# Optimization experiments

Hardware: AMD Instinct MI355X
Metric: run time of the kernel (lower is better)

The kernel has to match this reference:

```python
import jax, jax.numpy as jnp
import numpy as np

N, M, D, DE, H, G = 2048, 16, 512, 128, 8, 50
DH, DEH, NF = D // H, DE // H, 4  # head dims; 2**2 frames for 2D frame averaging
OPS = jnp.array([[-1., -1.], [-1., 1.], [1., -1.], [1., 1.]], dtype=jnp.float32)

def ln(x, eps=1e-5):
    m = x.mean(-1, keepdims=True)
    v = x.var(-1, keepdims=True)
    return (x - m) * jax.lax.rsqrt(v + eps)

def mlp2(x, w1, b1, w2, b2):
    # timm-style Mlp with norm_layer=LayerNorm: fc1 -> GELU -> LN -> fc2 (dropout=0)
    h = jax.nn.gelu(x @ w1 + b1, approximate=False)
    return ln(h) @ w2 + b2

def setup_inputs():
    key = jax.random.key(0)
    ks = iter(jax.random.split(key, 32))
    def w(shape):
        return jax.random.normal(next(ks), shape, jnp.float32) / float(np.sqrt(shape[0]))
    return dict(
        gene_exp=jax.random.uniform(next(ks), (N, G), jnp.float32),
        token_embs=jax.random.normal(next(ks), (N, D), jnp.float32),
        coords=jax.random.uniform(next(ks), (N, 2), jnp.float32) * 100.0,
        neighbor_indices=jax.random.randint(next(ks), (N, M), 0, N),
        w_qkv=w((D, 3 * D)), b_qkv=jnp.zeros((3 * D,), jnp.float32),
        wa1=w((2 * DH + DEH + G, D)), ba1=jnp.zeros((D,), jnp.float32),
        wa2=w((D, 1)), ba2=jnp.zeros((1,), jnp.float32),
        we1=w((3, DE)), be1=jnp.zeros((DE,), jnp.float32),
        we2=w((DE, DE)), be2=jnp.zeros((DE,), jnp.float32),
        wo1=w((D + DE, D)), bo1=jnp.zeros((D,), jnp.float32),
        wo2=w((D, D)), bo2=jnp.zeros((D,), jnp.float32),
        wm1=w((D, 4 * D)), bm1=jnp.zeros((4 * D,), jnp.float32),
        wm2=w((4 * D, D)), bm2=jnp.zeros((D,), jnp.float32),
        wg1=w((D, D)), bg1=jnp.zeros((D,), jnp.float32),
        wg2=w((D, G)), bg2=jnp.zeros((G,), jnp.float32),
    )

def reference(gene_exp, token_embs, coords, neighbor_indices, w_qkv, b_qkv, wa1, ba1, wa2, ba2, we1, be1, we2, be2, wo1, bo1, wo2, bo2, wm1, bm1, wm2, bm2, wg1, bg1, wg2, bg2):
    qkv = ln(token_embs) @ w_qkv + b_qkv
    q, k, v = jnp.split(qkv, 3, axis=-1)
    q, k, v = (t.reshape(N, H, DH) for t in (q, k, v))
    # --- frame averaging over neighbor point clouds (dim=2 -> 4 sign frames) ---
    radial = coords[neighbor_indices] - coords[:, None, :]            # [N,M,2]
    rnorm = jnp.linalg.norm(radial, axis=-1, keepdims=True)           # [N,M,1]
    Xc = radial - radial.mean(axis=1, keepdims=True)
    C = jnp.einsum('nmi,nmj->nij', Xc, Xc)                            # [N,2,2]
    _, V = jnp.linalg.eigh(jax.lax.stop_gradient(C))                  # eigh on detached cov (as in torch code)
    proj = jnp.einsum('nmj,nji->nmi', Xc, V)                          # [N,M,2]
    frame = OPS[None, :, None, :] * proj[:, None, :, :]               # [N,4,M,2]
    rn = jnp.broadcast_to(rnorm[:, None], (N, NF, M, 1))
    edge = mlp2(jnp.concatenate([frame, rn], axis=-1), we1, be1, we2, be2).mean(axis=1)  # [N,M,DE]
    # --- per-edge MLP attention ---
    gd = gene_exp[neighbor_indices] - gene_exp[:, None, :]            # [N,M,G]
    msg = jnp.concatenate([
        jnp.broadcast_to(q[:, None], (N, M, H, DH)),
        k[neighbor_indices],
        edge.reshape(N, M, H, DEH),
        jnp.broadcast_to(gd[:, :, None, :], (N, M, H, G)),
    ], axis=-1)                                                       # [N,M,H,2*DH+DEH+G]
    logits = mlp2(msg, wa1, ba1, wa2, ba2)[..., 0]                    # [N,M,H]
    attn = jax.nn.softmax(logits.transpose(0, 2, 1), axis=-1)         # [N,H,M]
    # --- context aggregation ---
    sc = jnp.einsum('nhm,nmhd->nhd', attn, v[neighbor_indices]).reshape(N, D)
    ec = jnp.einsum('nhm,nmhd->nhd', attn, edge.reshape(N, M, H, DEH)).reshape(N, DE)
    ctx = mlp2(jnp.concatenate([sc, ec], axis=-1), wo1, bo1, wo2, bo2)
    tok = token_embs + ctx
    tok = tok + mlp2(tok, wm1, bm1, wm2, bm2)
    # gene updater: Linear -> GELU -> LN -> Linear
    gene_out = mlp2(tok, wg1, bg1, wg2, bg2)
    return gene_out, tok
```

## Files before the change

kernel.cpp:

```cpp
#include <hip/hip_runtime.h>
#include <math.h>

#define NN 2048
#define MM 16
#define DD 512
#define DE 128
#define HH 8
#define GG 50
#define DH 64
#define DEH 16

typedef __attribute__((ext_vector_type(8))) short bf8_t;
typedef __attribute__((ext_vector_type(4))) float f4_t;
typedef __attribute__((ext_vector_type(2))) float f2_t;
typedef unsigned short us;

__device__ __forceinline__ void gload16(const us* g, us* l) {
    __builtin_amdgcn_global_load_lds(
        (const __attribute__((address_space(1))) unsigned int*)g,
        (__attribute__((address_space(3))) unsigned int*)l, 16, 0, 0);
}

__device__ __forceinline__ float gelu_f(float x) {
    float u = 1.5957691216f * fmaf(0.044715f * x, x * x, x);
    u = fminf(fmaxf(u, -30.f), 30.f);
    float e = __expf(u);
    float t = fmaf(-2.f, __builtin_amdgcn_rcpf(e + 1.f), 1.f);
    float hx = 0.5f * x;
    return fmaf(hx, t, hx);
}

__device__ __forceinline__ f2_t gelu2(f2_t x) {
    f2_t u = ((x * 0.044715f) * (x * x) + x) * 1.5957691216f;
    f2_t e1;
    e1.x = __expf(u.x) + 1.f;
    e1.y = __expf(u.y) + 1.f;
    f2_t r;
    r.x = __builtin_amdgcn_rcpf(e1.x);
    r.y = __builtin_amdgcn_rcpf(e1.y);
    f2_t t = r * (-2.f) + 1.f;
    f2_t hx = x * 0.5f;
    return hx * t + hx;
}

__device__ __forceinline__ float wsum(float v) {
#pragma unroll
    for (int o = 32; o; o >>= 1) v += __shfl_xor(v, o, 64);
    return v;
}

__device__ __forceinline__ us f2bf(float x) {
    union { float f; unsigned int u; } v;
    v.f = x;
    unsigned int r = v.u + 0x7FFFu + ((v.u >> 16) & 1u);
    return (us)(r >> 16);
}

__device__ __forceinline__ float bfu(unsigned int u) {
    union { unsigned int x; float f; } v;
    v.x = u;
    return v.f;
}
#define BF_LO(u) bfu((u) << 16)
#define BF_HI(u) bfu((u) & 0xFFFF0000u)
__device__ __forceinline__ float b2f(us u) { return bfu((unsigned int)u << 16); }

__global__ __launch_bounds__(256) void act_ln_kernel(float* __restrict__ outF,
                                                     us* __restrict__ outB,
                                                     const float* __restrict__ x,
                                                     int C, int do_gelu) {
    int row = blockIdx.x, tid = threadIdx.x;
    int nv = C >> 8;
    float v[8];
    float s = 0.f, ss = 0.f;
    for (int i = 0; i < nv; ++i) {
        float val = x[(size_t)row * C + tid + (i << 8)];
        if (do_gelu) val = gelu_f(val);
        v[i] = val;
        s += val;
        ss += val * val;
    }
    __shared__ float red[4][2];
    s = wsum(s);
    ss = wsum(ss);
    int wid = tid >> 6, lane = tid & 63;
    if (lane == 0) { red[wid][0] = s; red[wid][1] = ss; }
    __syncthreads();
    s = red[0][0] + red[1][0] + red[2][0] + red[3][0];
    ss = red[0][1] + red[1][1] + red[2][1] + red[3][1];
    float mean = s / (float)C;
    float var = ss / (float)C - mean * mean;
    float rs = rsqrtf(var + 1e-5f);
    for (int i = 0; i < nv; ++i) {
        float y = (v[i] - mean) * rs;
        size_t idx = (size_t)row * C + tid + (i << 8);
        if (outF) outF[idx] = y;
        if (outB) outB[idx] = f2bf(y);
    }
}

__global__ __launch_bounds__(256) void combine2ln_kernel(const float* __restrict__ pk,
                                                         const float* __restrict__ bias,
                                                         us* __restrict__ outB) {
    int row = blockIdx.x, tid = threadIdx.x;
    size_t b = (size_t)row * 512;
    float v0 = gelu_f(pk[b + tid] + pk[1048576 + b + tid] + bias[tid]);
    float v1 = gelu_f(pk[b + 256 + tid] + pk[1048576 + b + 256 + tid] + bias[256 + tid]);
    __shared__ float red[4][2];
    float s = wsum(v0 + v1);
    float ss = wsum(fmaf(v0, v0, v1 * v1));
    int wid = tid >> 6, lane = tid & 63;
    if (lane == 0) { red[wid][0] = s; red[wid][1] = ss; }
    __syncthreads();
    s = red[0][0] + red[1][0] + red[2][0] + red[3][0];
    ss = red[0][1] + red[1][1] + red[2][1] + red[3][1];
    float mean = s * (1.f / 512.f);
    float var = ss * (1.f / 512.f) - mean * mean;
    float rs = rsqrtf(var + 1e-5f);
    outB[b + tid] = f2bf((v0 - mean) * rs);
    outB[b + 256 + tid] = f2bf((v1 - mean) * rs);
}

__global__ __launch_bounds__(256) void combine2_kernel(const float* __restrict__ pk,
                                                       const float* __restrict__ bias,
                                                       const float* __restrict__ resid,
                                                       float* __restrict__ outF,
                                                       us* __restrict__ outB) {
    int idx = blockIdx.x * 256 + threadIdx.x;
    float v = pk[idx] + pk[idx + 1048576] + bias[idx & 511] + resid[idx];
    outF[idx] = v;
    outB[idx] = f2bf(v);
}

__global__ __launch_bounds__(256) void wm2_combine(const float* __restrict__ pk,
                                                   const float* __restrict__ bias,
                                                   const float* __restrict__ resid,
                                                   float* __restrict__ outF,
                                                   us* __restrict__ outB) {
    int idx = blockIdx.x * 256 + threadIdx.x;
    float v = pk[idx] + pk[idx + 1048576] + pk[idx + 2097152] + pk[idx + 3145728] +
              bias[idx & 511] + resid[idx];
    outF[idx] = v;
    outB[idx] = f2bf(v);
}

__global__ __launch_bounds__(256) void wg2_combine(const float* __restrict__ pk,
                                                   const float* __restrict__ bias,
                                                   float* __restrict__ outF) {
    int idx = blockIdx.x * 256 + threadIdx.x;
    if (idx >= 102400) return;
    float v = pk[idx] + pk[idx + 102400] + pk[idx + 204800] + pk[idx + 307200] +
              bias[idx % 50];
    outF[idx] = v;
}

__global__ __launch_bounds__(256) void lnproj_kernel(const float* __restrict__ te,
                                                     us* __restrict__ x_ln_bf,
                                                     const float* __restrict__ coords,
                                                     const int* __restrict__ nbr,
                                                     float* __restrict__ projs,
                                                     float* __restrict__ rns) {
    int tid = threadIdx.x;
    if (blockIdx.x < 2048) {
        int row = blockIdx.x;
        float v0 = te[(size_t)row * 512 + tid];
        float v1 = te[(size_t)row * 512 + 256 + tid];
        __shared__ float red[4][2];
        float s = wsum(v0 + v1);
        float ss = wsum(fmaf(v0, v0, v1 * v1));
        int wid = tid >> 6, lane = tid & 63;
        if (lane == 0) { red[wid][0] = s; red[wid][1] = ss; }
        __syncthreads();
        s = red[0][0] + red[1][0] + red[2][0] + red[3][0];
        ss = red[0][1] + red[1][1] + red[2][1] + red[3][1];
        float mean = s * (1.f / 512.f);
        float var = ss * (1.f / 512.f) - mean * mean;
        float rs = rsqrtf(var + 1e-5f);
        x_ln_bf[(size_t)row * 512 + tid] = f2bf((v0 - mean) * rs);
        x_ln_bf[(size_t)row * 512 + 256 + tid] = f2bf((v1 - mean) * rs);
        return;
    }
    int node = (blockIdx.x - 2048) * 16 + (tid >> 4);
    int m = tid & 15;
    float cx = coords[node * 2], cy = coords[node * 2 + 1];
    int j = nbr[node * 16 + m];
    float rx = coords[j * 2] - cx;
    float ry = coords[j * 2 + 1] - cy;
    float rn = sqrtf(rx * rx + ry * ry);
    float mx = rx, my = ry;
#pragma unroll
    for (int o = 8; o; o >>= 1) { mx += __shfl_xor(mx, o, 16); my += __shfl_xor(my, o, 16); }
    mx *= 0.0625f;
    my *= 0.0625f;
    float xcx = rx - mx, xcy = ry - my;
    float sxx = xcx * xcx, sxy = xcx * xcy, syy = xcy * xcy;
#pragma unroll
    for (int o = 8; o; o >>= 1) {
        sxx += __shfl_xor(sxx, o, 16);
        sxy += __shfl_xor(sxy, o, 16);
        syy += __shfl_xor(syy, o, 16);
    }
    double a = (double)sxx, b = (double)sxy, c = (double)syy;
    double diff = 0.5 * (a - c);
    double disc = sqrt(diff * diff + b * b);
    double l2 = 0.5 * (a + c) + disc;
    double v2x = b, v2y = l2 - a;
    double nn2 = sqrt(v2x * v2x + v2y * v2y);
    if (nn2 < 1e-30) { v2x = (a >= c) ? 1.0 : 0.0; v2y = 1.0 - v2x; nn2 = 1.0; }
    v2x /= nn2;
    v2y /= nn2;
    double v1x = -v2y, v1y = v2x;
    int row = node * 16 + m;
    projs[row * 2] = (float)((double)xcx * v1x + (double)xcy * v1y);
    projs[row * 2 + 1] = (float)((double)xcx * v2x + (double)xcy * v2y);
    rns[row] = rn;
}

struct TCJob {
    const float* src;
    us* dst;
    int K, N, Kld, b0;
};
struct TC11 {
    TCJob j[11];
    int acc_end;
    const float* wa1_s;
    us* wesT_d;
    const float* gene_s;
    us* gene_d;
};

__global__ __launch_bounds__(256) void tcast_all(TC11 P) {
    __shared__ float tile[32][33];
    int b = blockIdx.x;
    if (b >= P.acc_end) {
        int lb = b - P.acc_end;
        if (lb < 64) {
            int idx = lb * 256 + threadIdx.x;
            int c = idx >> 5, t = idx & 31;
            P.wesT_d[idx] = (t < 16) ? f2bf(P.wa1_s[(size_t)(128 + t) * 512 + c]) : (us)0;
        } else {
            int idx = (lb - 64) * 256 + threadIdx.x;
            int r = idx >> 6, c = idx & 63;
            P.gene_d[idx] = (c < 50) ? f2bf(P.gene_s[r * 50 + c]) : (us)0;
        }
        return;
    }
    int ji = 0;
#pragma unroll
    for (int i = 1; i < 11; ++i)
        if (b >= P.j[i].b0) ji = i;
    const float* W = P.j[ji].src;
    us* Wt = P.j[ji].dst;
    int K = P.j[ji].K, N = P.j[ji].N, Kld = P.j[ji].Kld;
    int lb = b - P.j[ji].b0;
    int nbx = (N + 31) >> 5;
    int n0 = (lb % nbx) * 32, k0 = (lb / nbx) * 32;
    int tx = threadIdx.x & 31, ty = threadIdx.x >> 5;
#pragma unroll
    for (int p = 0; p < 4; ++p) {
        int k = k0 + ty + p * 8;
        tile[ty + p * 8][tx] = (k < K && n0 + tx < N) ? W[(size_t)k * N + n0 + tx] : 0.f;
    }
    __syncthreads();
#pragma unroll
    for (int p = 0; p < 4; ++p) {
        int n = n0 + ty + p * 8;
        if (n < N && k0 + tx < Kld) Wt[(size_t)n * Kld + k0 + tx] = f2bf(tile[tx][ty + p * 8]);
    }
}

struct GJob {
    const us* A;
    const us* Bt;
    const float* bias;
    const float* resid;
    const float* residH;
    float* outF;
    us* outB;
    us* outB2;
    us* outB3;
    int M, Kstride, nkt, N, Nout, b0;
};
struct GJobs {
    GJob j[4];
    int nj;
};

__global__ __launch_bounds__(256) void gemm_bf16_kernel(GJobs P) {
    __shared__ us As[2][128 * 64];
    __shared__ us Bs[2][128 * 64];
    int b = blockIdx.x;
    int ji = 0;
#pragma unroll
    for (int i = 1; i < 4; ++i)
        if (i < P.nj && b >= P.j[i].b0) ji = i;
    const us* A = P.j[ji].A;
    const us* Bt = P.j[ji].Bt;
    int Kst = P.j[ji].Kstride, nkt = P.j[ji].nkt;
    int Nn = P.j[ji].N, Nout = P.j[ji].Nout;
    int lb = b - P.j[ji].b0;
    int ncol = Nn >> 7;
    int col0 = (lb % ncol) << 7, row0 = (lb / ncol) << 7;

    int tid = threadIdx.x;
    int lane = tid & 63;
    int w = tid >> 6;
    int wr = w >> 1, wc = w & 1;
    f4_t acc[4][4];
#pragma unroll
    for (int a = 0; a < 4; ++a)
#pragma unroll
        for (int bb = 0; bb < 4; ++bb) {
            acc[a][bb][0] = 0.f; acc[a][bb][1] = 0.f;
            acc[a][bb][2] = 0.f; acc[a][bb][3] = 0.f;
        }

    auto stage = [&](int buf, int kt) {
#pragma unroll
        for (int p = 0; p < 4; ++p) {
            int id = p * 256 + tid;
            int r = id >> 3, cch = id & 7;
            int kc = cch ^ (r & 7);
            int wb = p * 256 + (tid & 192);
            gload16(A + (size_t)(row0 + r) * Kst + kt + kc * 8, As[buf] + wb * 8);
            gload16(Bt + (size_t)(col0 + r) * Kst + kt + kc * 8, Bs[buf] + wb * 8);
        }
    };

    stage(0, 0);
    __syncthreads();
    for (int t = 0; t < nkt; ++t) {
        int cur = t & 1;
        if (t + 1 < nkt) stage(cur ^ 1, (t + 1) << 6);
#pragma unroll
        for (int kk = 0; kk < 2; ++kk) {
            bf8_t af[4], bfr[4];
            int kslot = kk * 4 + (lane >> 4);
#pragma unroll
            for (int mi = 0; mi < 4; ++mi) {
                int r = wr * 64 + mi * 16 + (lane & 15);
                af[mi] = *(const bf8_t*)((char*)As[cur] + r * 128 + ((kslot ^ (r & 7)) * 16));
            }
#pragma unroll
            for (int ni = 0; ni < 4; ++ni) {
                int r = wc * 64 + ni * 16 + (lane & 15);
                bfr[ni] = *(const bf8_t*)((char*)Bs[cur] + r * 128 + ((kslot ^ (r & 7)) * 16));
            }
#pragma unroll
            for (int mi = 0; mi < 4; ++mi)
#pragma unroll
                for (int ni = 0; ni < 4; ++ni)
                    acc[mi][ni] = __builtin_amdgcn_mfma_f32_16x16x32_bf16(
                        af[mi], bfr[ni], acc[mi][ni], 0, 0, 0);
        }
        __syncthreads();
    }
    const float* bias = P.j[ji].bias;
    const float* resid = P.j[ji].resid;
    const float* residH = P.j[ji].residH;
    float* outF = P.j[ji].outF;
    us* outB = P.j[ji].outB;
    us* outB2 = P.j[ji].outB2;
    us* outB3 = P.j[ji].outB3;
    int cr = lane >> 4, cc = lane & 15;
#pragma unroll
    for (int mi = 0; mi < 4; ++mi)
#pragma unroll
        for (int ni = 0; ni < 4; ++ni) {
            int col = col0 + wc * 64 + ni * 16 + cc;
            if (col >= Nout) continue;
            float bv = bias ? bias[col] : 0.f;
#pragma unroll
            for (int j = 0; j < 4; ++j) {
                int row = row0 + wr * 64 + mi * 16 + cr * 4 + j;
                float v = acc[mi][ni][j] + bv;
                if (resid) v += resid[(size_t)row * Nout + col];
                if (residH) v += residH[(size_t)(row >> 3) * Nout + col];
                if (outF) outF[(size_t)row * Nout + col] = v;
                if (outB) {
                    if (outB2) {
                        int seg = col >> 9, cl = col & 511;
                        us* dst = seg == 0 ? outB : (seg == 1 ? outB2 : outB3);
                        dst[(size_t)row * 512 + cl] = f2bf(v);
                    } else {
                        outB[(size_t)row * Nout + col] = f2bf(v);
                    }
                }
            }
        }
}

__global__ __launch_bounds__(256) void frame_mlp1_kernel(const float* __restrict__ projs,
                                                         const float* __restrict__ rns,
                                                         const float* __restrict__ we1,
                                                         const float* __restrict__ be1,
                                                         us* __restrict__ u) {
    int row = blockIdx.x * 4 + (threadIdx.x >> 6);
    int lane = threadIdx.x & 63;
    float px = projs[row * 2], py = projs[row * 2 + 1], rn = rns[row];
    int c0 = lane, c1 = lane + 64;
    float w10a = we1[c0], w11a = we1[128 + c0], w12a = we1[256 + c0], b1a = be1[c0];
    float w10b = we1[c1], w11b = we1[128 + c1], w12b = we1[256 + c1], b1b = be1[c1];
    float acc0 = 0.f, acc1 = 0.f;
    const float opsx[4] = {-1.f, -1.f, 1.f, 1.f};
    const float opsy[4] = {-1.f, 1.f, -1.f, 1.f};
#pragma unroll
    for (int f = 0; f < 4; ++f) {
        float fx = opsx[f] * px, fy = opsy[f] * py;
        float h0 = gelu_f(fmaf(fx, w10a, fmaf(fy, w11a, fmaf(rn, w12a, b1a))));
        float h1 = gelu_f(fmaf(fx, w10b, fmaf(fy, w11b, fmaf(rn, w12b, b1b))));
        float s = wsum(h0 + h1);
        float ss = wsum(fmaf(h0, h0, h1 * h1));
        float mean = s * (1.f / 128.f);
        float var = ss * (1.f / 128.f) - mean * mean;
        float rs = rsqrtf(var + 1e-5f);
        acc0 += (h0 - mean) * rs;
        acc1 += (h1 - mean) * rs;
    }
    u[(size_t)row * 128 + c0] = f2bf(0.25f * acc0);
    u[(size_t)row * 128 + c1] = f2bf(0.25f * acc1);
}

__global__ __launch_bounds__(256) void logits_fused_kernel(
    const us* __restrict__ qpb,
    const us* __restrict__ k2b,
    const us* __restrict__ gepb,
    const us* __restrict__ edgeb,
    const us* __restrict__ wesT,
    const us* __restrict__ wa1kT,
    const int* __restrict__ nbr,
    const float* __restrict__ wa2,
    const float* __restrict__ ba2,
    const us* __restrict__ v2b,
    us* __restrict__ scec) {
    __shared__ us Es[2048 + 32];
    __shared__ us qmg[8 * 520];
    __shared__ us gepj[16 * 512];
    __shared__ float wa2s[512];
    __shared__ float lgs[128];
    __shared__ float attn[128];
    __shared__ float sinv[8];
    __shared__ int jns[16];
    int n = blockIdx.x, tid = threadIdx.x;
    int lane = tid & 63;
    float swv = 0.f;
#pragma unroll
    for (int i = 0; i < 8; ++i) swv += wa2[lane + 64 * i];
    float sw = wsum(swv);
    float ba2v = ba2[0];
    {
        const uint* s2 = (const uint*)(edgeb + (size_t)n * 2048);
        uint* d2 = (uint*)Es;
        for (int i = tid; i < 1040; i += 256) d2[i] = s2[i];
        const uint* s3 = (const uint*)(qpb + (size_t)n * 4096);
        const uint* s4 = (const uint*)(gepb + (size_t)n * 512);
        uint* d3 = (uint*)qmg;
        for (int i = tid; i < 2048; i += 256) {
            uint q = s3[i], g = s4[i & 255];
            float lo = BF_LO(q) - BF_LO(g), hi = BF_HI(q) - BF_HI(g);
            d3[(i >> 8) * 260 + (i & 255)] = ((uint)f2bf(hi) << 16) | (uint)f2bf(lo);
        }
        uint* d5 = (uint*)gepj;
#pragma unroll 4
        for (int p = 0; p < 16; ++p) {
            int j = nbr[n * 16 + p];
            d5[p * 256 + tid] = ((const uint*)(gepb + (size_t)j * 512))[tid];
        }
        for (int i = tid; i < 512; i += 256) wa2s[i] = wa2[i];
        if (tid < 16) jns[tid] = nbr[n * 16 + tid];
    }
    __syncthreads();

    int cc = lane & 15, cr = lane >> 4;
    int w = tid >> 6;
#pragma unroll
    for (int mt = 0; mt < 2; ++mt) {
        int mh = w * 32 + mt * 16 + cc;
        int m = mh >> 3, h = mh & 7;
        int j8h = jns[m] * 8 + h;
        const us* qrow = qmg + h * 520;
        const us* gjrow = gepj + m * 512;
        bf8_t bfr = *(const bf8_t*)((const char*)Es + mh * 32 + cr * 16);
        bf8_t bk0 = *(const bf8_t*)(k2b + (size_t)j8h * 64 + cr * 8);
        bf8_t bk1 = *(const bf8_t*)(k2b + (size_t)j8h * 64 + 32 + cr * 8);
        f2_t s2v = {0.f, 0.f}, ss2 = {0.f, 0.f}, sd2 = {0.f, 0.f};
#pragma unroll 4
        for (int ct = 0; ct < 32; ++ct) {
            int chb = ct * 16 + cr * 4;
            bf8_t afw = *(const bf8_t*)(wesT + (ct * 16 + cc) * 32 + cr * 8);
            bf8_t afk0 = *(const bf8_t*)(wa1kT + (ct * 16 + cc) * 64 + cr * 8);
            bf8_t afk1 = *(const bf8_t*)(wa1kT + (ct * 16 + cc) * 64 + 32 + cr * 8);
            f4_t z = {0.f, 0.f, 0.f, 0.f};
            f4_t ep = __builtin_amdgcn_mfma_f32_16x16x32_bf16(afk0, bk0, z, 0, 0, 0);
            ep = __builtin_amdgcn_mfma_f32_16x16x32_bf16(afk1, bk1, ep, 0, 0, 0);
            ep = __builtin_amdgcn_mfma_f32_16x16x32_bf16(afw, bfr, ep, 0, 0, 0);
            uint2 qp4 = *(const uint2*)(qrow + chb);
            uint2 gj4 = *(const uint2*)(gjrow + chb);
            float4 w4 = *(const float4*)(wa2s + chb);
            f2_t ep01 = {ep[0], ep[1]}, ep23 = {ep[2], ep[3]};
            f2_t q01 = {BF_LO(qp4.x), BF_HI(qp4.x)};
            f2_t q23 = {BF_LO(qp4.y), BF_HI(qp4.y)};
            f2_t g01v = {BF_LO(gj4.x), BF_HI(gj4.x)};
            f2_t g23v = {BF_LO(gj4.y), BF_HI(gj4.y)};
            f2_t g01 = gelu2(ep01 + q01 + g01v);
            f2_t g23 = gelu2(ep23 + q23 + g23v);
            s2v += g01;
            s2v += g23;
            ss2 = g01 * g01 + ss2;
            ss2 = g23 * g23 + ss2;
            f2_t w01 = {w4.x, w4.y}, w23 = {w4.z, w4.w};
            sd2 = g01 * w01 + sd2;
            sd2 = g23 * w23 + sd2;
        }
        float s = s2v.x + s2v.y, ss = ss2.x + ss2.y, sd = sd2.x + sd2.y;
        s += __shfl_xor(s, 16, 64);
        s += __shfl_xor(s, 32, 64);
        ss += __shfl_xor(ss, 16, 64);
        ss += __shfl_xor(ss, 32, 64);
        sd += __shfl_xor(sd, 16, 64);
        sd += __shfl_xor(sd, 32, 64);
        if (cr == 0) {
            float mean = s * (1.f / 512.f);
            float var = ss * (1.f / 512.f) - mean * mean;
            lgs[mh] = (sd - mean * sw) * rsqrtf(var + 1e-5f) + ba2v;
        }
    }
    __syncthreads();
    if (tid < 128) {
        int h = tid & 7;
        float mx = lgs[h];
#pragma unroll
        for (int mm = 1; mm < 16; ++mm) mx = fmaxf(mx, lgs[mm * 8 + h]);
        attn[tid] = __expf(lgs[tid] - mx);
    }
    __syncthreads();
    if (tid < 8) {
        float se = 0.f;
#pragma unroll
        for (int mm = 0; mm < 16; ++mm) se += attn[mm * 8 + tid];
        sinv[tid] = 1.f / se;
    }
    __syncthreads();
    for (int c = tid; c < 640; c += 256) {
        float acc = 0.f;
        int h;
        if (c < 512) {
            h = c >> 6;
            int t = c & 63;
#pragma unroll
            for (int m = 0; m < 16; ++m)
                acc = fmaf(attn[m * 8 + h], b2f(v2b[(size_t)jns[m] * 512 + h * 64 + t]), acc);
        } else {
            int d = c - 512;
            h = d >> 4;
            int t = d & 15;
#pragma unroll
            for (int m = 0; m < 16; ++m)
                acc = fmaf(attn[m * 8 + h], b2f(Es[m * 128 + h * 16 + t]), acc);
        }
        scec[(size_t)n * 640 + c] = f2bf(acc * sinv[h]);
    }
}

extern "C" void kernel_launch(void* const* d_in, const int* in_sizes, int n_in,
                              void* d_out, int out_size, void* d_ws, size_t ws_size,
                              hipStream_t stream) {
    const float* gene_exp = (const float*)d_in[0];
    const float* token_embs = (const float*)d_in[1];
    const float* coords = (const float*)d_in[2];
    const int* nbr = (const int*)d_in[3];
    const float* w_qkv = (const float*)d_in[4];
    const float* b_qkv = (const float*)d_in[5];
    const float* wa1 = (const float*)d_in[6];
    const float* ba1 = (const float*)d_in[7];
    const float* wa2 = (const float*)d_in[8];
    const float* ba2 = (const float*)d_in[9];
    const float* we1 = (const float*)d_in[10];
    const float* be1 = (const float*)d_in[11];
    const float* we2 = (const float*)d_in[12];
    const float* be2 = (const float*)d_in[13];
    const float* wo1 = (const float*)d_in[14];
    const float* bo1 = (const float*)d_in[15];
    const float* wo2 = (const float*)d_in[16];
    const float* bo2 = (const float*)d_in[17];
    const float* wm1 = (const float*)d_in[18];
    const float* bm1 = (const float*)d_in[19];
    const float* wm2 = (const float*)d_in[20];
    const float* bm2 = (const float*)d_in[21];
    const float* wg1 = (const float*)d_in[22];
    const float* bg1 = (const float*)d_in[23];
    const float* wg2 = (const float*)d_in[24];
    const float* bg2 = (const float*)d_in[25];

    float* out = (float*)d_out;
    float* gene_out = out;
    float* tok_out = out + 2048 * 50;

    float* ws = (float*)d_ws;
    size_t o = 0;
    auto alloc = [&](size_t nf) {
        float* p = ws + o;
        o += nf;
        return p;
    };
    us* x_ln_bf = (us*)alloc((size_t)2048 * 512 / 2);
    us* q2b = (us*)alloc((size_t)16384 * 64 / 2);
    us* k2b = (us*)alloc((size_t)16384 * 64 / 2);
    us* v2b = (us*)alloc((size_t)2048 * 512 / 2);
    us* qpb = (us*)alloc((size_t)16384 * 512 / 2);
    us* gepb = (us*)alloc((size_t)2048 * 512 / 2);
    us* edgeb = (us*)alloc(((size_t)2048 * 2048 + 32) / 2);
    us* scec_bf = (us*)alloc((size_t)2048 * 640 / 2);
    us* buf1_bf = (us*)alloc((size_t)2048 * 512 / 2);
    float* buf2 = alloc((size_t)2048 * 2048);
    us* buf2_bf = (us*)alloc((size_t)2048 * 2048 / 2);
    float* tok1 = alloc((size_t)2048 * 512);
    us* tok1_bf = (us*)alloc((size_t)2048 * 512 / 2);
    us* tokout_bf = (us*)alloc((size_t)2048 * 512 / 2);
    us* u_bf = (us*)alloc((size_t)32768 * 128 / 2);
    float* projs = alloc((size_t)32768 * 2);
    float* rns = alloc((size_t)32768);
    us* gene_bf = (us*)alloc((size_t)2048 * 64 / 2);
    float* pk4 = alloc((size_t)4 * 2048 * 512);
    us* qkvT = (us*)alloc((size_t)1536 * 512 / 2);
    us* wa1qT = (us*)alloc((size_t)512 * 64 / 2);
    us* wa1kT = (us*)alloc((size_t)512 * 64 / 2);
    us* wa1gT = (us*)alloc((size_t)512 * 64 / 2);
    us* we2T = (us*)alloc((size_t)128 * 128 / 2);
    us* wo1T = (us*)alloc((size_t)512 * 640 / 2);
    us* wo2T = (us*)alloc((size_t)512 * 512 / 2);
    us* wm1T = (us*)alloc((size_t)2048 * 512 / 2);
    us* wm2T = (us*)alloc((size_t)512 * 2048 / 2);
    us* wg1T = (us*)alloc((size_t)512 * 512 / 2);
    us* wg2T = (us*)alloc((size_t)128 * 512 / 2);
    us* wesT = (us*)alloc((size_t)512 * 32 / 2);
    if (o * sizeof(float) > ws_size) return;

    auto mkjob = [](const us* A, const us* Bt, const float* bias, const float* resid,
                    const float* residH, float* outF, us* outB, us* outB2, us* outB3,
                    int M, int Kstride, int nkt, int N, int Nout, int b0) {
        GJob j;
        j.A = A; j.Bt = Bt; j.bias = bias; j.resid = resid; j.residH = residH;
        j.outF = outF; j.outB = outB; j.outB2 = outB2; j.outB3 = outB3;
        j.M = M; j.Kstride = Kstride; j.nkt = nkt; j.N = N; j.Nout = Nout; j.b0 = b0;
        return j;
    };
    auto G1 = [&](const us* A, const us* Bt, const float* bias, const float* resid,
                  const float* residH, float* outF, us* outB, int M, int K, int N,
                  int Nout) {
        GJobs P;
        P.nj = 1;
        P.j[0] = mkjob(A, Bt, bias, resid, residH, outF, outB, nullptr, nullptr,
                       M, K, K >> 6, N, Nout, 0);
        gemm_bf16_kernel<<<(N / 128) * (M / 128), 256, 0, stream>>>(P);
    };
    auto Gsk2 = [&](const us* A, const us* Bt, int M, int K, int N) {
        GJobs P;
        P.nj = 2;
        int half = K >> 1;
        int blk = (N / 128) * (M / 128);
        P.j[0] = mkjob(A, Bt, nullptr, nullptr, nullptr, pk4, nullptr, nullptr, nullptr,
                       M, K, half >> 6, N, N, 0);
        P.j[1] = mkjob(A + half, Bt + half, nullptr, nullptr, nullptr, pk4 + 1048576,
                       nullptr, nullptr, nullptr, M, K, half >> 6, N, N, blk);
        gemm_bf16_kernel<<<2 * blk, 256, 0, stream>>>(P);
    };

    hipMemsetAsync(wg2T, 0, (size_t)128 * 512 * 2, stream);
    {
        TC11 P;
        auto set = [&](int i, const float* s, us* d, int K, int N, int Kld, int& acc) {
            P.j[i] = {s, d, K, N, Kld, acc};
            acc += ((N + 31) / 32) * ((Kld + 31) / 32);
        };
        int acc = 0;
        set(0, w_qkv, qkvT, 512, 1536, 512, acc);
        set(1, wa1, wa1qT, 64, 512, 64, acc);
        set(2, wa1 + 64 * 512, wa1kT, 64, 512, 64, acc);
        set(3, we2, we2T, 128, 128, 128, acc);
        set(4, wo1, wo1T, 640, 512, 640, acc);
        set(5, wo2, wo2T, 512, 512, 512, acc);
        set(6, wm1, wm1T, 512, 2048, 512, acc);
        set(7, wm2, wm2T, 2048, 512, 2048, acc);
        set(8, wg1, wg1T, 512, 512, 512, acc);
        set(9, wa1 + 144 * 512, wa1gT, 50, 512, 64, acc);
        set(10, wg2, wg2T, 512, 50, 512, acc);
        P.acc_end = acc;
        P.wa1_s = wa1;
        P.wesT_d = wesT;
        P.gene_s = gene_exp;
        P.gene_d = gene_bf;
        tcast_all<<<acc + 64 + 512, 256, 0, stream>>>(P);
    }

    lnproj_kernel<<<2048 + 128, 256, 0, stream>>>(token_embs, x_ln_bf, coords, nbr,
                                                  projs, rns);
    frame_mlp1_kernel<<<8192, 256, 0, stream>>>(projs, rns, we1, be1, u_bf);
    {
        GJobs P;
        P.nj = 2;
        P.j[0] = mkjob(x_ln_bf, qkvT, b_qkv, nullptr, nullptr, nullptr, q2b, k2b, v2b,
                       2048, 512, 8, 1536, 1536, 0);
        P.j[1] = mkjob(gene_bf, wa1gT, nullptr, nullptr, nullptr, nullptr, gepb, nullptr,
                       nullptr, 2048, 64, 1, 512, 512, 192);
        gemm_bf16_kernel<<<256, 256, 0, stream>>>(P);
    }
    {
        GJobs P;
        P.nj = 2;
        P.j[0] = mkjob(q2b, wa1qT, ba1, nullptr, nullptr, nullptr, qpb, nullptr, nullptr,
                       16384, 64, 1, 512, 512, 0);
        P.j[1] = mkjob(u_bf, we2T, be2, nullptr, nullptr, nullptr, edgeb, nullptr,
                       nullptr, 32768, 128, 2, 128, 128, 512);
        gemm_bf16_kernel<<<768, 256, 0, stream>>>(P);
    }
    logits_fused_kernel<<<2048, 256, 0, stream>>>(qpb, k2b, gepb, edgeb, wesT, wa1kT,
                                                  nbr, wa2, ba2, v2b, scec_bf);
    Gsk2(scec_bf, wo1T, 2048, 640, 512);
    combine2ln_kernel<<<2048, 256, 0, stream>>>(pk4, bo1, buf1_bf);
    Gsk2(buf1_bf, wo2T, 2048, 512, 512);
    combine2_kernel<<<4096, 256, 0, stream>>>(pk4, bo2, token_embs, tok1, tok1_bf);
    G1(tok1_bf, wm1T, bm1, nullptr, nullptr, buf2, nullptr, 2048, 512, 2048, 2048);
    act_ln_kernel<<<2048, 256, 0, stream>>>(nullptr, buf2_bf, buf2, 2048, 1);
    {
        GJobs P;
        P.nj = 4;
#pragma unroll
        for (int s = 0; s < 4; ++s)
            P.j[s] = mkjob(buf2_bf + s * 512, wm2T + s * 512, nullptr, nullptr, nullptr,
                           pk4 + (size_t)s * 1048576, nullptr, nullptr, nullptr,
                           2048, 2048, 8, 512, 512, s * 64);
        gemm_bf16_kernel<<<256, 256, 0, stream>>>(P);
        wm2_combine<<<4096, 256, 0, stream>>>(pk4, bm2, tok1, tok_out, tokout_bf);
    }
    Gsk2(tokout_bf, wg1T, 2048, 512, 512);
    combine2ln_kernel<<<2048, 256, 0, stream>>>(pk4, bg1, buf1_bf);
    {
        GJobs P;
        P.nj = 4;
#pragma unroll
        for (int s = 0; s < 4; ++s)
            P.j[s] = mkjob(buf1_bf + s * 128, wg2T + s * 128, nullptr, nullptr, nullptr,
                           pk4 + (size_t)s * 102400, nullptr, nullptr, nullptr,
                           2048, 512, 2, 128, 50, s * 16);
        gemm_bf16_kernel<<<64, 256, 0, stream>>>(P);
        wg2_combine<<<400, 256, 0, stream>>>(pk4, bg2, gene_out);
    }
}
```

Measured before the change: 377.3 us.

## Precompute per-node K·Wa1k plus gene projection instead of per-edge MFMA

Precomputes k projected through the key slice of wa1, with the gene-expression projection added, as a per-(node,head) 512-wide bf16 table (kgb) in the batched GEMM launch. The logits kernel then gathers the neighbour's row instead of doing two extra MFMAs per tile and staging neighbour gene projections in shared memory. This cuts per-edge matrix work and shared memory, at the cost of a larger GEMM, a 16 MB intermediate written and then gathered, and an extra fp32 gep buffer.

```diff
diff --git a/kernel.cpp b/kernel.cpp
--- a/kernel.cpp
+++ b/kernel.cpp
@@ -424,11 +424,10 @@
 
 __global__ __launch_bounds__(256) void logits_fused_kernel(
     const us* __restrict__ qpb,
-    const us* __restrict__ k2b,
+    const us* __restrict__ kg,
     const us* __restrict__ gepb,
     const us* __restrict__ edgeb,
     const us* __restrict__ wesT,
-    const us* __restrict__ wa1kT,
     const int* __restrict__ nbr,
     const float* __restrict__ wa2,
     const float* __restrict__ ba2,
@@ -436,7 +435,6 @@
     us* __restrict__ scec) {
     __shared__ us Es[2048 + 32];
     __shared__ us qmg[8 * 520];
-    __shared__ us gepj[16 * 512];
     __shared__ float wa2s[512];
     __shared__ float lgs[128];
     __shared__ float attn[128];
@@ -461,12 +459,6 @@
             float lo = BF_LO(q) - BF_LO(g), hi = BF_HI(q) - BF_HI(g);
             d3[(i >> 8) * 260 + (i & 255)] = ((uint)f2bf(hi) << 16) | (uint)f2bf(lo);
         }
-        uint* d5 = (uint*)gepj;
-#pragma unroll 4
-        for (int p = 0; p < 16; ++p) {
-            int j = nbr[n * 16 + p];
-            d5[p * 256 + tid] = ((const uint*)(gepb + (size_t)j * 512))[tid];
-        }
         for (int i = tid; i < 512; i += 256) wa2s[i] = wa2[i];
         if (tid < 16) jns[tid] = nbr[n * 16 + tid];
     }
@@ -479,32 +471,26 @@
         int mh = w * 32 + mt * 16 + cc;
         int m = mh >> 3, h = mh & 7;
         int j8h = jns[m] * 8 + h;
+        const us* kgrow = kg + (size_t)j8h * 512;
         const us* qrow = qmg + h * 520;
-        const us* gjrow = gepj + m * 512;
         bf8_t bfr = *(const bf8_t*)((const char*)Es + mh * 32 + cr * 16);
-        bf8_t bk0 = *(const bf8_t*)(k2b + (size_t)j8h * 64 + cr * 8);
-        bf8_t bk1 = *(const bf8_t*)(k2b + (size_t)j8h * 64 + 32 + cr * 8);
         f2_t s2v = {0.f, 0.f}, ss2 = {0.f, 0.f}, sd2 = {0.f, 0.f};
 #pragma unroll 4
         for (int ct = 0; ct < 32; ++ct) {
             int chb = ct * 16 + cr * 4;
-            bf8_t afw = *(const bf8_t*)(wesT + (ct * 16 + cc) * 32 + cr * 8);
-            bf8_t afk0 = *(const bf8_t*)(wa1kT + (ct * 16 + cc) * 64 + cr * 8);
-            bf8_t afk1 = *(const bf8_t*)(wa1kT + (ct * 16 + cc) * 64 + 32 + cr * 8);
+            bf8_t af = *(const bf8_t*)(wesT + (ct * 16 + cc) * 32 + cr * 8);
             f4_t z = {0.f, 0.f, 0.f, 0.f};
-            f4_t ep = __builtin_amdgcn_mfma_f32_16x16x32_bf16(afk0, bk0, z, 0, 0, 0);
-            ep = __builtin_amdgcn_mfma_f32_16x16x32_bf16(afk1, bk1, ep, 0, 0, 0);
-            ep = __builtin_amdgcn_mfma_f32_16x16x32_bf16(afw, bfr, ep, 0, 0, 0);
+            f4_t ep = __builtin_amdgcn_mfma_f32_16x16x32_bf16(af, bfr, z, 0, 0, 0);
+            uint2 kg4 = *(const uint2*)(kgrow + chb);
             uint2 qp4 = *(const uint2*)(qrow + chb);
-            uint2 gj4 = *(const uint2*)(gjrow + chb);
             float4 w4 = *(const float4*)(wa2s + chb);
             f2_t ep01 = {ep[0], ep[1]}, ep23 = {ep[2], ep[3]};
             f2_t q01 = {BF_LO(qp4.x), BF_HI(qp4.x)};
             f2_t q23 = {BF_LO(qp4.y), BF_HI(qp4.y)};
-            f2_t g01v = {BF_LO(gj4.x), BF_HI(gj4.x)};
-            f2_t g23v = {BF_LO(gj4.y), BF_HI(gj4.y)};
-            f2_t g01 = gelu2(ep01 + q01 + g01v);
-            f2_t g23 = gelu2(ep23 + q23 + g23v);
+            f2_t k01 = {BF_LO(kg4.x), BF_HI(kg4.x)};
+            f2_t k23 = {BF_LO(kg4.y), BF_HI(kg4.y)};
+            f2_t g01 = gelu2(ep01 + q01 + k01);
+            f2_t g23 = gelu2(ep23 + q23 + k23);
             s2v += g01;
             s2v += g23;
             ss2 = g01 * g01 + ss2;
@@ -609,6 +595,8 @@
     us* k2b = (us*)alloc((size_t)16384 * 64 / 2);
     us* v2b = (us*)alloc((size_t)2048 * 512 / 2);
     us* qpb = (us*)alloc((size_t)16384 * 512 / 2);
+    us* kgb = (us*)alloc((size_t)16384 * 512 / 2);
+    float* gep = alloc((size_t)2048 * 512);
     us* gepb = (us*)alloc((size_t)2048 * 512 / 2);
     us* edgeb = (us*)alloc(((size_t)2048 * 2048 + 32) / 2);
     us* scec_bf = (us*)alloc((size_t)2048 * 640 / 2);
@@ -702,21 +690,23 @@
         P.nj = 2;
         P.j[0] = mkjob(x_ln_bf, qkvT, b_qkv, nullptr, nullptr, nullptr, q2b, k2b, v2b,
                        2048, 512, 8, 1536, 1536, 0);
-        P.j[1] = mkjob(gene_bf, wa1gT, nullptr, nullptr, nullptr, nullptr, gepb, nullptr,
+        P.j[1] = mkjob(gene_bf, wa1gT, nullptr, nullptr, nullptr, gep, gepb, nullptr,
                        nullptr, 2048, 64, 1, 512, 512, 192);
         gemm_bf16_kernel<<<256, 256, 0, stream>>>(P);
     }
     {
         GJobs P;
-        P.nj = 2;
+        P.nj = 3;
         P.j[0] = mkjob(q2b, wa1qT, ba1, nullptr, nullptr, nullptr, qpb, nullptr, nullptr,
                        16384, 64, 1, 512, 512, 0);
-        P.j[1] = mkjob(u_bf, we2T, be2, nullptr, nullptr, nullptr, edgeb, nullptr,
-                       nullptr, 32768, 128, 2, 128, 128, 512);
-        gemm_bf16_kernel<<<768, 256, 0, stream>>>(P);
-    }
-    logits_fused_kernel<<<2048, 256, 0, stream>>>(qpb, k2b, gepb, edgeb, wesT, wa1kT,
-                                                  nbr, wa2, ba2, v2b, scec_bf);
+        P.j[1] = mkjob(k2b, wa1kT, nullptr, nullptr, gep, nullptr, kgb, nullptr, nullptr,
+                       16384, 64, 1, 512, 512, 512);
+        P.j[2] = mkjob(u_bf, we2T, be2, nullptr, nullptr, nullptr, edgeb, nullptr,
+                       nullptr, 32768, 128, 2, 128, 128, 1024);
+        gemm_bf16_kernel<<<1280, 256, 0, stream>>>(P);
+    }
+    logits_fused_kernel<<<2048, 256, 0, stream>>>(qpb, kgb, gepb, edgeb, wesT, nbr,
+                                                  wa2, ba2, v2b, scec_bf);
     Gsk2(scec_bf, wo1T, 2048, 640, 512);
     combine2ln_kernel<<<2048, 256, 0, stream>>>(pk4, bo1, buf1_bf);
     Gsk2(buf1_bf, wo2T, 2048, 512, 512);
```

After: 338.0 us. -10.4%, faster.
